# Kernel optimization log

Hardware: AMD Instinct MI355X
Metric: run time of the kernel (lower is better)

Reference implementation:

```python
import jax, jax.numpy as jnp
import numpy as np
import math

B, S, D = 8, 2048, 512
X_SCALE = 0.02  # keep exp(x @ x^T) finite (raw unit-variance dots ~N(0, D) would overflow exp)


def setup_inputs() -> dict:
    key = jax.random.key(0)
    kx, km = jax.random.split(key)
    x = jax.random.normal(kx, (B, S, D), dtype=jnp.float32) * X_SCALE
    mask = jax.random.randint(km, (B, S, S), 0, 2, dtype=jnp.int32)
    return {"x": x, "mask": mask}


def reference(x, mask):
    # scores = exp(x @ x^T) / sqrt(D)  -- non-standard: exp BEFORE scaling/softmax
    scores = jnp.exp(jnp.einsum("bqd,bkd->bqk", x, x)) / math.sqrt(x.shape[-1])
    scores = jnp.where(mask == 0, jnp.float32(-1e9), scores)
    p_attn = jax.nn.softmax(scores, axis=-1)  # dropout is identity in eval mode
    output = jnp.einsum("bqk,bkd->bqd", p_attn, x)
    # flatten=True path: sum over sequence dim
    return output.sum(axis=1), p_attn
```

## Files before the change

kernel.cpp:

```cpp
#include <hip/hip_runtime.h>
#include <cstdint>
#include <cstddef>

#define B_ 8
#define S_ 2048
#define D_ 512

typedef __attribute__((ext_vector_type(8))) short short8;
typedef __attribute__((ext_vector_type(4))) float f32x4;

__device__ inline unsigned short f2bf(float f) {
  unsigned u = __float_as_uint(f);
  u += 0x7FFFu + ((u >> 16) & 1u);
  return (unsigned short)(u >> 16);
}

__global__ __launch_bounds__(256) void prep_kernel(
    const float* __restrict__ x, unsigned short* __restrict__ xb,
    const int* __restrict__ mask, unsigned char* __restrict__ bm) {
  const int tid = blockIdx.x * blockDim.x + threadIdx.x;
  const int nth = gridDim.x * blockDim.x;
  const float4* x4 = (const float4*)x;
  ushort4* o4 = (ushort4*)xb;
  for (int i = tid; i < B_ * S_ * D_ / 4; i += nth) {
    float4 v = x4[i];
    ushort4 o;
    o.x = f2bf(v.x); o.y = f2bf(v.y); o.z = f2bf(v.z); o.w = f2bf(v.w);
    o4[i] = o;
  }
  for (int j = tid; j < B_ * S_ * S_ / 8; j += nth) {
    const int4* m4 = (const int4*)mask + 2 * (size_t)j;
    int4 a = m4[0], b = m4[1];
    unsigned byte = (unsigned)(a.x != 0) | ((unsigned)(a.y != 0) << 1) |
                    ((unsigned)(a.z != 0) << 2) | ((unsigned)(a.w != 0) << 3) |
                    ((unsigned)(b.x != 0) << 4) | ((unsigned)(b.y != 0) << 5) |
                    ((unsigned)(b.z != 0) << 6) | ((unsigned)(b.w != 0) << 7);
    bm[j] = (unsigned char)byte;
  }
}

#define GLDS(g, l) __builtin_amdgcn_global_load_lds( \
    (const __attribute__((address_space(1))) void*)(g), \
    (__attribute__((address_space(3))) void*)(l), 16, 0, 0)

__global__ __launch_bounds__(256) void gemm_u_kernel(
    const unsigned short* __restrict__ xb, const unsigned char* __restrict__ bm,
    float* __restrict__ ubuf, float* __restrict__ Z) {
  __shared__ unsigned short At[128 * 64];
  __shared__ unsigned short Bt[128 * 64];
  __shared__ unsigned char mrow[128 * 16];

  const int logical = (blockIdx.x & 7) * 256 + (blockIdx.x >> 3);
  const int b = logical >> 8;
  const int qt = (logical >> 4) & 15;
  const int kt = logical & 15;
  const int tid = threadIdx.x;
  const int wid = tid >> 6;
  const int lane = tid & 63;
  const int l15 = lane & 15;
  const int l7 = lane & 7;
  const int lg = lane >> 4;

  const unsigned short* xbat = xb + (size_t)b * S_ * D_;
  const unsigned short* aglob = xbat + (size_t)qt * 128 * D_;
  const unsigned short* bglob = xbat + (size_t)kt * 128 * D_;

  if (tid < 128) {
    *(uint4*)&mrow[tid * 16] =
        *(const uint4*)(bm + ((size_t)b * S_ + qt * 128 + tid) * (S_ / 8) +
                        kt * 16);
  }

  f32x4 acc[4][4] = {};

  const int wr = (wid >> 1) * 64;
  const int wc = (wid & 1) * 64;

  for (int k0 = 0; k0 < D_; k0 += 64) {
    __syncthreads();
    #pragma unroll
    for (int i = 0; i < 4; i++) {
      int c = i * 256 + tid;
      int row = c >> 3;
      int col8 = (c & 7) ^ (row & 7);
      GLDS(aglob + row * D_ + k0 + col8 * 8, &At[c * 8]);
      GLDS(bglob + row * D_ + k0 + col8 * 8, &Bt[c * 8]);
    }
    __syncthreads();
    #pragma unroll
    for (int ks8 = 0; ks8 < 8; ks8 += 4) {
      const int kc8 = ks8 + lg;
      short8 av[4], bv[4];
      #pragma unroll
      for (int m = 0; m < 4; m++) {
        int row = wr + m * 16 + l15;
        av[m] = *(const short8*)&At[row * 64 + ((kc8 ^ l7) << 3)];
      }
      #pragma unroll
      for (int n = 0; n < 4; n++) {
        int row = wc + n * 16 + l15;
        bv[n] = *(const short8*)&Bt[row * 64 + ((kc8 ^ l7) << 3)];
      }
      #pragma unroll
      for (int m = 0; m < 4; m++)
        #pragma unroll
        for (int n = 0; n < 4; n++)
          acc[m][n] = __builtin_amdgcn_mfma_f32_16x16x32_bf16(
              av[m], bv[n], acc[m][n], 0, 0, 0);
    }
  }
  __syncthreads();

  const float inv_sqrt_d = 0.04419417382415922f;
  float* ubat = ubuf + (size_t)b * S_ * S_;
  float* Zb = Z + b * S_;

  #pragma unroll
  for (int m = 0; m < 4; m++) {
    float rsum[4] = {0.f, 0.f, 0.f, 0.f};
    #pragma unroll
    for (int r = 0; r < 4; r++) {
      const int trow = wr + m * 16 + lg * 4 + r;
      const uint2 mb = *(const uint2*)&mrow[trow * 16 + (wc >> 3)];
      #pragma unroll
      for (int n = 0; n < 4; n++) {
        const int idx = n * 16 + l15;
        const unsigned bit = (n < 2) ? (mb.x >> idx) : (mb.y >> (idx - 32));
        float u = 0.0f;
        if (bit & 1u)
          u = __expf(__expf(acc[m][n][r]) * inv_sqrt_d);
        ubat[(size_t)(qt * 128 + trow) * S_ + kt * 128 + wc + n * 16 + l15] = u;
        rsum[r] += u;
      }
    }
    #pragma unroll
    for (int r = 0; r < 4; r++) {
      float v = rsum[r];
      v += __shfl_xor(v, 1);
      v += __shfl_xor(v, 2);
      v += __shfl_xor(v, 4);
      v += __shfl_xor(v, 8);
      if (l15 == 0)
        atomicAdd(&Zb[qt * 128 + wr + m * 16 + lg * 4 + r], v);
    }
  }
}

__global__ __launch_bounds__(256) void norm_kernel(
    float* __restrict__ p, const float* __restrict__ Z, float* __restrict__ cs) {
  const int b = blockIdx.y;
  const int qc = blockIdx.x;
  const int t = threadIdx.x;
  float4* prow = (float4*)(p + ((size_t)b * S_ + qc * 16) * S_);
  const float* Zb = Z + b * S_ + qc * 16;
  float4 a0 = {0.f, 0.f, 0.f, 0.f};
  float4 a1 = {0.f, 0.f, 0.f, 0.f};
  for (int r = 0; r < 16; r++) {
    float invZ = 1.0f / Zb[r];
    float4 u0 = prow[r * 512 + t];
    float4 u1 = prow[r * 512 + t + 256];
    u0.x *= invZ; u0.y *= invZ; u0.z *= invZ; u0.w *= invZ;
    u1.x *= invZ; u1.y *= invZ; u1.z *= invZ; u1.w *= invZ;
    prow[r * 512 + t] = u0;
    prow[r * 512 + t + 256] = u1;
    a0.x += u0.x; a0.y += u0.y; a0.z += u0.z; a0.w += u0.w;
    a1.x += u1.x; a1.y += u1.y; a1.z += u1.z; a1.w += u1.w;
  }
  float* csb = cs + b * S_;
  atomicAdd(&csb[4 * t + 0], a0.x);
  atomicAdd(&csb[4 * t + 1], a0.y);
  atomicAdd(&csb[4 * t + 2], a0.z);
  atomicAdd(&csb[4 * t + 3], a0.w);
  atomicAdd(&csb[1024 + 4 * t + 0], a1.x);
  atomicAdd(&csb[1024 + 4 * t + 1], a1.y);
  atomicAdd(&csb[1024 + 4 * t + 2], a1.z);
  atomicAdd(&csb[1024 + 4 * t + 3], a1.w);
}

__global__ __launch_bounds__(512) void out_kernel(
    const float* __restrict__ x, const float* __restrict__ cs,
    float* __restrict__ out) {
  const int b = blockIdx.y;
  const int k0 = blockIdx.x * 32;
  const int d = threadIdx.x;
  const float* xbat = x + (size_t)b * S_ * D_;
  const float* csb = cs + b * S_;
  float acc = 0.f;
  #pragma unroll 8
  for (int k = k0; k < k0 + 32; k++)
    acc += csb[k] * xbat[(size_t)k * D_ + d];
  atomicAdd(&out[b * D_ + d], acc);
}

extern "C" void kernel_launch(void* const* d_in, const int* in_sizes, int n_in,
                              void* d_out, int out_size, void* d_ws, size_t ws_size,
                              hipStream_t stream) {
  const float* x = (const float*)d_in[0];
  const int* mask = (const int*)d_in[1];
  float* out = (float*)d_out;
  float* p = out + B_ * D_;

  unsigned short* xb = (unsigned short*)d_ws;
  unsigned char* bm = (unsigned char*)d_ws + (size_t)B_ * S_ * D_ * 2;
  float* Z = (float*)(bm + (size_t)B_ * S_ * (S_ / 8));
  float* cs = Z + B_ * S_;

  hipMemsetAsync(Z, 0, 2 * (size_t)B_ * S_ * sizeof(float), stream);
  hipMemsetAsync(out, 0, (size_t)B_ * D_ * sizeof(float), stream);

  prep_kernel<<<2048, 256, 0, stream>>>(x, xb, mask, bm);
  gemm_u_kernel<<<2048, 256, 0, stream>>>(xb, bm, p, Z);
  norm_kernel<<<dim3(S_ / 16, B_), 256, 0, stream>>>(p, Z, cs);
  out_kernel<<<dim3(S_ / 32, B_), 512, 0, stream>>>(x, cs, out);
}
```

Before: 374.1 us.

## Fuse mask bit-packing into GEMM, restructure norm and output reduction kernels

Mask bit-packing moves out of the prep kernel and into the GEMM prologue. Each block now reads its own 128x128 int tile of the mask directly, which removes a separate pass and the round trip through the packed bitmask buffer. The norm kernel is reorganised so each block owns a 128-column strip and half of the rows. It uses nontemporal loads and stores and reduces in shared memory, which cuts the column-sum atomics sharply. The output kernel changes to 256 threads with two outputs per thread and longer k chunks. The GEMM also gets a min-blocks occupancy hint, which may raise register pressure.

```diff
diff --git a/kernel.cpp b/kernel.cpp
--- a/kernel.cpp
+++ b/kernel.cpp
@@ -15,36 +15,33 @@
   return (unsigned short)(u >> 16);
 }
 
-__global__ __launch_bounds__(256) void prep_kernel(
-    const float* __restrict__ x, unsigned short* __restrict__ xb,
-    const int* __restrict__ mask, unsigned char* __restrict__ bm) {
-  const int tid = blockIdx.x * blockDim.x + threadIdx.x;
-  const int nth = gridDim.x * blockDim.x;
+__global__ __launch_bounds__(256) void convert_kernel(
+    const float* __restrict__ x, unsigned short* __restrict__ xb) {
   const float4* x4 = (const float4*)x;
   ushort4* o4 = (ushort4*)xb;
-  for (int i = tid; i < B_ * S_ * D_ / 4; i += nth) {
+  const int nth = gridDim.x * blockDim.x;
+  for (int i = blockIdx.x * blockDim.x + threadIdx.x; i < B_ * S_ * D_ / 4;
+       i += nth) {
     float4 v = x4[i];
     ushort4 o;
     o.x = f2bf(v.x); o.y = f2bf(v.y); o.z = f2bf(v.z); o.w = f2bf(v.w);
     o4[i] = o;
   }
-  for (int j = tid; j < B_ * S_ * S_ / 8; j += nth) {
-    const int4* m4 = (const int4*)mask + 2 * (size_t)j;
-    int4 a = m4[0], b = m4[1];
-    unsigned byte = (unsigned)(a.x != 0) | ((unsigned)(a.y != 0) << 1) |
-                    ((unsigned)(a.z != 0) << 2) | ((unsigned)(a.w != 0) << 3) |
-                    ((unsigned)(b.x != 0) << 4) | ((unsigned)(b.y != 0) << 5) |
-                    ((unsigned)(b.z != 0) << 6) | ((unsigned)(b.w != 0) << 7);
-    bm[j] = (unsigned char)byte;
-  }
 }
 
 #define GLDS(g, l) __builtin_amdgcn_global_load_lds( \
     (const __attribute__((address_space(1))) void*)(g), \
     (__attribute__((address_space(3))) void*)(l), 16, 0, 0)
 
-__global__ __launch_bounds__(256) void gemm_u_kernel(
-    const unsigned short* __restrict__ xb, const unsigned char* __restrict__ bm,
+__device__ inline unsigned pack8(int4 a, int4 b) {
+  return (unsigned)(a.x != 0) | ((unsigned)(a.y != 0) << 1) |
+         ((unsigned)(a.z != 0) << 2) | ((unsigned)(a.w != 0) << 3) |
+         ((unsigned)(b.x != 0) << 4) | ((unsigned)(b.y != 0) << 5) |
+         ((unsigned)(b.z != 0) << 6) | ((unsigned)(b.w != 0) << 7);
+}
+
+__global__ __launch_bounds__(256, 4) void gemm_u_kernel(
+    const unsigned short* __restrict__ xb, const int* __restrict__ mask,
     float* __restrict__ ubuf, float* __restrict__ Z) {
   __shared__ unsigned short At[128 * 64];
   __shared__ unsigned short Bt[128 * 64];
@@ -60,21 +57,39 @@
   const int l15 = lane & 15;
   const int l7 = lane & 7;
   const int lg = lane >> 4;
+  const int wr = (wid >> 1) * 64;
+  const int wc = (wid & 1) * 64;
+  const float inv_sqrt_d = 0.04419417382415922f;
 
   const unsigned short* xbat = xb + (size_t)b * S_ * D_;
   const unsigned short* aglob = xbat + (size_t)qt * 128 * D_;
   const unsigned short* bglob = xbat + (size_t)kt * 128 * D_;
 
-  if (tid < 128) {
-    *(uint4*)&mrow[tid * 16] =
-        *(const uint4*)(bm + ((size_t)b * S_ + qt * 128 + tid) * (S_ / 8) +
-                        kt * 16);
+  {
+    const int trow = tid >> 1;
+    const int half = tid & 1;
+    const int4* mg = (const int4*)(mask + ((size_t)b * S_ + qt * 128 + trow) * S_ +
+                                   kt * 128 + half * 64);
+    unsigned lo = 0, hi = 0;
+    #pragma unroll
+    for (int c4 = 0; c4 < 4; c4++) {
+      int4 a = mg[c4 * 4 + 0];
+      int4 bb = mg[c4 * 4 + 1];
+      int4 c = mg[c4 * 4 + 2];
+      int4 d = mg[c4 * 4 + 3];
+      unsigned by0 = pack8(a, bb);
+      unsigned by1 = pack8(c, d);
+      if (c4 < 2) {
+        lo |= (by0 << (c4 * 16)) | (by1 << (c4 * 16 + 8));
+      } else {
+        hi |= (by0 << ((c4 - 2) * 16)) | (by1 << ((c4 - 2) * 16 + 8));
+      }
+    }
+    uint2 pk; pk.x = lo; pk.y = hi;
+    *(uint2*)&mrow[trow * 16 + half * 8] = pk;
   }
 
   f32x4 acc[4][4] = {};
-
-  const int wr = (wid >> 1) * 64;
-  const int wc = (wid & 1) * 64;
 
   for (int k0 = 0; k0 < D_; k0 += 64) {
     __syncthreads();
@@ -111,7 +126,6 @@
   }
   __syncthreads();
 
-  const float inv_sqrt_d = 0.04419417382415922f;
   float* ubat = ubuf + (size_t)b * S_ * S_;
   float* Zb = Z + b * S_;
 
@@ -149,47 +163,57 @@
 __global__ __launch_bounds__(256) void norm_kernel(
     float* __restrict__ p, const float* __restrict__ Z, float* __restrict__ cs) {
   const int b = blockIdx.y;
-  const int qc = blockIdx.x;
+  const int cc = blockIdx.x >> 1;
+  const int rh = blockIdx.x & 1;
   const int t = threadIdx.x;
-  float4* prow = (float4*)(p + ((size_t)b * S_ + qc * 16) * S_);
-  const float* Zb = Z + b * S_ + qc * 16;
-  float4 a0 = {0.f, 0.f, 0.f, 0.f};
-  float4 a1 = {0.f, 0.f, 0.f, 0.f};
-  for (int r = 0; r < 16; r++) {
-    float invZ = 1.0f / Zb[r];
-    float4 u0 = prow[r * 512 + t];
-    float4 u1 = prow[r * 512 + t + 256];
-    u0.x *= invZ; u0.y *= invZ; u0.z *= invZ; u0.w *= invZ;
-    u1.x *= invZ; u1.y *= invZ; u1.z *= invZ; u1.w *= invZ;
-    prow[r * 512 + t] = u0;
-    prow[r * 512 + t + 256] = u1;
-    a0.x += u0.x; a0.y += u0.y; a0.z += u0.z; a0.w += u0.w;
-    a1.x += u1.x; a1.y += u1.y; a1.z += u1.z; a1.w += u1.w;
-  }
-  float* csb = cs + b * S_;
-  atomicAdd(&csb[4 * t + 0], a0.x);
-  atomicAdd(&csb[4 * t + 1], a0.y);
-  atomicAdd(&csb[4 * t + 2], a0.z);
-  atomicAdd(&csb[4 * t + 3], a0.w);
-  atomicAdd(&csb[1024 + 4 * t + 0], a1.x);
-  atomicAdd(&csb[1024 + 4 * t + 1], a1.y);
-  atomicAdd(&csb[1024 + 4 * t + 2], a1.z);
-  atomicAdd(&csb[1024 + 4 * t + 3], a1.w);
-}
-
-__global__ __launch_bounds__(512) void out_kernel(
+  const int s = t & 31;
+  const int g = t >> 5;
+  const int c0 = cc * 128;
+  __shared__ float red[8][128];
+
+  f32x4* p4 = (f32x4*)(p + (size_t)b * S_ * S_);
+  const float* Zb = Z + b * S_;
+  float s0 = 0.f, s1 = 0.f, s2 = 0.f, s3 = 0.f;
+  const int qbase = rh * 1024 + g;
+  for (int i = 0; i < 128; i++) {
+    const int q = qbase + i * 8;
+    const float invZ = 1.0f / Zb[q];
+    f32x4* addr = &p4[(size_t)q * (S_ / 4) + (c0 >> 2) + s];
+    f32x4 u = __builtin_nontemporal_load(addr);
+    u *= invZ;
+    __builtin_nontemporal_store(u, addr);
+    s0 += u.x; s1 += u.y; s2 += u.z; s3 += u.w;
+  }
+  red[g][s * 4 + 0] = s0;
+  red[g][s * 4 + 1] = s1;
+  red[g][s * 4 + 2] = s2;
+  red[g][s * 4 + 3] = s3;
+  __syncthreads();
+  if (t < 128) {
+    float v = 0.f;
+    #pragma unroll
+    for (int gg = 0; gg < 8; gg++) v += red[gg][t];
+    atomicAdd(&cs[b * S_ + c0 + t], v);
+  }
+}
+
+__global__ __launch_bounds__(256) void out_kernel(
     const float* __restrict__ x, const float* __restrict__ cs,
     float* __restrict__ out) {
-  const int b = blockIdx.y;
-  const int k0 = blockIdx.x * 32;
-  const int d = threadIdx.x;
+  const int b = blockIdx.x & 7;
+  const int k0 = (blockIdx.x >> 3) * 64;
+  const int tid = threadIdx.x;
   const float* xbat = x + (size_t)b * S_ * D_;
   const float* csb = cs + b * S_;
-  float acc = 0.f;
-  #pragma unroll 8
-  for (int k = k0; k < k0 + 32; k++)
-    acc += csb[k] * xbat[(size_t)k * D_ + d];
-  atomicAdd(&out[b * D_ + d], acc);
+  float a0 = 0.f, a1 = 0.f;
+  #pragma unroll 4
+  for (int k = k0; k < k0 + 64; k++) {
+    float c = csb[k];
+    a0 += c * xbat[(size_t)k * D_ + tid];
+    a1 += c * xbat[(size_t)k * D_ + tid + 256];
+  }
+  atomicAdd(&out[b * D_ + tid], a0);
+  atomicAdd(&out[b * D_ + tid + 256], a1);
 }
 
 extern "C" void kernel_launch(void* const* d_in, const int* in_sizes, int n_in,
@@ -201,15 +225,14 @@
   float* p = out + B_ * D_;
 
   unsigned short* xb = (unsigned short*)d_ws;
-  unsigned char* bm = (unsigned char*)d_ws + (size_t)B_ * S_ * D_ * 2;
-  float* Z = (float*)(bm + (size_t)B_ * S_ * (S_ / 8));
+  float* Z = (float*)((char*)d_ws + (size_t)B_ * S_ * D_ * 2);
   float* cs = Z + B_ * S_;
 
   hipMemsetAsync(Z, 0, 2 * (size_t)B_ * S_ * sizeof(float), stream);
   hipMemsetAsync(out, 0, (size_t)B_ * D_ * sizeof(float), stream);
 
-  prep_kernel<<<2048, 256, 0, stream>>>(x, xb, mask, bm);
-  gemm_u_kernel<<<2048, 256, 0, stream>>>(xb, bm, p, Z);
-  norm_kernel<<<dim3(S_ / 16, B_), 256, 0, stream>>>(p, Z, cs);
-  out_kernel<<<dim3(S_ / 32, B_), 512, 0, stream>>>(x, cs, out);
-}
+  convert_kernel<<<1024, 256, 0, stream>>>(x, xb);
+  gemm_u_kernel<<<2048, 256, 0, stream>>>(xb, mask, p, Z);
+  norm_kernel<<<dim3(32, B_), 256, 0, stream>>>(p, Z, cs);
+  out_kernel<<<256, 256, 0, stream>>>(x, cs, out);
+}
```

Measured after the change: 362.9 us. 3.0% less time.
